# Performance work log

Hardware: AMD Instinct MI355X
Metric: run time of the kernel (lower is better)

The kernel has to match this reference:

```python
import jax, jax.numpy as jnp
import numpy as np


def setup_inputs() -> dict:
    key = jax.random.key(0)
    ks = jax.random.split(key, 6)
    B, N, D, H, W = 8, 16, 128, 64, 64
    x = jax.random.normal(ks[0], (B, N, D, H, W), dtype=jnp.float32)
    mask = jax.random.randint(ks[1], (B, N, H, W), 0, 2, dtype=jnp.int32)
    s = 1.0 / np.sqrt(D)
    Wq = jax.random.normal(ks[2], (D, D), dtype=jnp.float32) * s
    bq = jax.random.normal(ks[3], (D,), dtype=jnp.float32) * s
    Wk = jax.random.normal(ks[4], (D, D), dtype=jnp.float32) * s
    bk = jax.random.normal(ks[5], (D,), dtype=jnp.float32) * s
    return {"x": x, "mask": mask, "Wq": Wq, "bq": bq, "Wk": Wk, "bk": bk}


def reference(x, mask, Wq, bq, Wk, bk):
    B, N, D, H, W = x.shape
    K = H * W
    # (B, N, K, D) token view of spatial grid
    xr = jnp.transpose(x, (0, 1, 3, 4, 2)).reshape(B, N, K, D)
    m = mask.reshape(B, N, K, 1).astype(x.dtype)
    valid_count = jnp.sum(m, axis=2, keepdims=True)          # (B, N, 1, 1)
    mean_x = jnp.sum(xr * m, axis=2, keepdims=True) / valid_count  # (B, N, 1, D)
    # Linear layers: y = x @ W^T + b (torch convention)
    query = mean_x @ Wq.T + bq                               # (B, N, 1, D)
    keys = xr @ Wk.T + bk                                    # (B, N, K, D)
    attn = jnp.einsum('bnqd,bnkd->bnqk', query, keys)        # (B, N, 1, K)
    neg_inf = jnp.array(-jnp.inf, dtype=attn.dtype)
    attn = jnp.where(m.reshape(B, N, 1, K) == 0, neg_inf, attn)
    attn = jax.nn.softmax(attn / jnp.sqrt(jnp.asarray(D, attn.dtype)), axis=-1)
    pooled = jnp.einsum('bnqk,bnkd->bnqd', attn, xr)         # (B, N, 1, D)
    return pooled[:, :, 0, :]                                 # (B, N, D)
```

## Files before the change

### kernel.cpp

```cpp
#include <hip/hip_runtime.h>
#include <math.h>

#define G 128
#define D 128
#define K 4096
#define CK 64
#define PAD 1


__global__ __launch_bounds__(256) void k1_mean(const float* __restrict__ x,
                                               const int* __restrict__ mask,
                                               float* __restrict__ meanacc,
                                               float* __restrict__ oacc,
                                               float* __restrict__ denom) {
  __shared__ float mf[K];
  const int g = blockIdx.x >> 5;
  const int s = blockIdx.x & 31;
  const int tid = threadIdx.x;
  if (s == 0) {
    if (tid < D) oacc[g * D + tid] = 0.0f;
    if (tid == D) denom[g] = 0.0f;
  }
  const int4* m4 = (const int4*)(mask + (size_t)g * K);
  for (int i = tid; i < K / 4; i += 256) {
    int4 mi = m4[i];
    *(float4*)&mf[4 * i] =
        make_float4((float)mi.x, (float)mi.y, (float)mi.z, (float)mi.w);
  }
  __syncthreads();
  const int wid = tid >> 6, lane = tid & 63;
  const int d = s * 4 + wid;
  const float4* x4 = (const float4*)(x + ((size_t)g * D + d) * K);
  const float4* mf4 = (const float4*)mf;
  float4 acc = make_float4(0.f, 0.f, 0.f, 0.f);
#pragma unroll
  for (int it = 0; it < K / 256; ++it) {
    float4 a = x4[it * 64 + lane];
    float4 m = mf4[it * 64 + lane];
    acc.x += a.x * m.x;
    acc.y += a.y * m.y;
    acc.z += a.z * m.z;
    acc.w += a.w * m.w;
  }
  float sum = acc.x + acc.y + acc.z + acc.w;
#pragma unroll
  for (int o = 32; o > 0; o >>= 1) sum += __shfl_down(sum, o, 64);
  if (lane == 0) meanacc[g * D + d] = sum;
}

__global__ __launch_bounds__(128) void k2_query(
    const float* __restrict__ meanacc, const int* __restrict__ mask,
    const float* __restrict__ Wq, const float* __restrict__ bq,
    const float* __restrict__ Wk, const float* __restrict__ bk,
    float* __restrict__ qt, float* __restrict__ cvec) {
  __shared__ float mean_s[D], query_s[D], red[D];
  const int g = blockIdx.x, t = threadIdx.x;
  const int4* m4 = (const int4*)(mask + (size_t)g * K);
  int csum = 0;
  for (int i = t; i < K / 4; i += 128) {
    int4 v = m4[i];
    csum += v.x + v.y + v.z + v.w;
  }
  red[t] = (float)csum;
  __syncthreads();
  for (int o = 64; o > 0; o >>= 1) {
    if (t < o) red[t] += red[t + o];
    __syncthreads();
  }
  const float cnt = red[0];
  mean_s[t] = meanacc[g * D + t] / cnt;
  __syncthreads();
  float q = bq[t];
  for (int d = 0; d < D; ++d) q += mean_s[d] * Wq[t * D + d];
  query_s[t] = q;
  __syncthreads();
  red[t] = q * bk[t];
  __syncthreads();
  for (int o = 64; o > 0; o >>= 1) {
    if (t < o) red[t] += red[t + o];
    __syncthreads();
  }
  if (t == 0) cvec[g] = red[0];
  float qq = 0.f;
  for (int d = 0; d < D; ++d) qq += query_s[d] * Wk[d * D + t];
  qt[g * D + t] = qq;
}

__global__ __launch_bounds__(256) void k3_fused(
    const float* __restrict__ x, const int* __restrict__ mask,
    const float* __restrict__ qt, const float* __restrict__ cvec,
    float* __restrict__ oacc, float* __restrict__ denom) {
  __shared__ float xs[D][CK + PAD];
  __shared__ float qs[D];
  __shared__ float part_l[4][CK];
  __shared__ float wsm[CK];
  __shared__ float red[256];
  const int g = blockIdx.x >> 6;
  const int k0 = (blockIdx.x & 63) * CK;
  const int tid = threadIdx.x;
  if (tid < D) qs[tid] = qt[g * D + tid];
  const float4* xg = (const float4*)(x + (size_t)g * D * K + k0);
  for (int i = tid; i < D * (CK / 4); i += 256) {
    int d = i >> 4, j = i & 15;
    float4 v = xg[(size_t)d * (K / 4) + j];
    xs[d][4 * j + 0] = v.x;
    xs[d][4 * j + 1] = v.y;
    xs[d][4 * j + 2] = v.z;
    xs[d][4 * j + 3] = v.w;
  }
  __syncthreads();
  {
    const int k = tid & 63, p = tid >> 6;
    float s = 0.f;
#pragma unroll 8
    for (int d = p * 32; d < p * 32 + 32; ++d) s += qs[d] * xs[d][k];
    part_l[p][k] = s;
  }
  __syncthreads();
  if (tid < CK) {
    const float scale = 0.08838834764831845f;
    float l = (part_l[0][tid] + part_l[1][tid] + part_l[2][tid] +
               part_l[3][tid] + cvec[g]) * scale;
    float w = mask[(size_t)g * K + k0 + tid] ? __expf(l) : 0.f;
    wsm[tid] = w;
#pragma unroll
    for (int o = 32; o > 0; o >>= 1) w += __shfl_down(w, o, 64);
    if (tid == 0) atomicAdd(denom + g, w);
  }
  __syncthreads();
  {
    const int d = tid & 127, h = tid >> 7;
    float a = 0.f;
#pragma unroll 8
    for (int i = h * 32; i < h * 32 + 32; ++i) a += wsm[i] * xs[d][i];
    red[tid] = a;
  }
  __syncthreads();
  if (tid < D) atomicAdd(oacc + g * D + tid, red[tid] + red[tid + 128]);
}

__global__ __launch_bounds__(256) void k4_norm(const float* __restrict__ oacc,
                                               const float* __restrict__ denom,
                                               float* __restrict__ out) {
  int i = blockIdx.x * 256 + threadIdx.x;
  out[i] = oacc[i] / denom[i >> 7];
}

extern "C" void kernel_launch(void* const* d_in, const int* in_sizes, int n_in,
                              void* d_out, int out_size, void* d_ws,
                              size_t ws_size, hipStream_t stream) {
  const float* x = (const float*)d_in[0];
  const int* mask = (const int*)d_in[1];
  const float* Wq = (const float*)d_in[2];
  const float* bq = (const float*)d_in[3];
  const float* Wk = (const float*)d_in[4];
  const float* bk = (const float*)d_in[5];
  float* out = (float*)d_out;

  float* ws = (float*)d_ws;
  float* meanacc = ws;
  float* qt = ws + G * D;
  float* cvec = ws + 2 * G * D;
  float* oacc = ws + 2 * G * D + G;
  float* denom = ws + 3 * G * D + G;

  k1_mean<<<G * 32, 256, 0, stream>>>(x, mask, meanacc, oacc, denom);
  k2_query<<<G, 128, 0, stream>>>(meanacc, mask, Wq, bq, Wk, bk, qt, cvec);
  k3_fused<<<G * (K / CK), 256, 0, stream>>>(x, mask, qt, cvec, oacc, denom);
  k4_norm<<<(G * D) / 256, 256, 0, stream>>>(oacc, denom, out);
}
```

Baseline: 449.1 us.

## Fuse all four stages into one persistent cooperative kernel with work-stealing counters

Replaces the four separate launches with one persistent cooperative kernel. Blocks claim work items from atomic counters: first the masked mean reduction, then the per-group query projection run by the last finisher of each group, then the chunked attention-pooling items, which spin on a per-group ready flag. The last chunk of each group writes the normalized output. This removes kernel launch gaps and the separate normalize pass, and lets the phases of different groups overlap. In exchange it adds atomic and spin-wait overhead, a memset, and an occupancy query on the host on every launch.

```diff
diff --git a/kernel.cpp b/kernel.cpp
--- a/kernel.cpp
+++ b/kernel.cpp
@@ -5,145 +5,194 @@
 #define D 128
 #define K 4096
 #define CK 64
-#define PAD 1
-
-
-__global__ __launch_bounds__(256) void k1_mean(const float* __restrict__ x,
-                                               const int* __restrict__ mask,
-                                               float* __restrict__ meanacc,
-                                               float* __restrict__ oacc,
-                                               float* __restrict__ denom) {
-  __shared__ float mf[K];
-  const int g = blockIdx.x >> 5;
-  const int s = blockIdx.x & 31;
-  const int tid = threadIdx.x;
-  if (s == 0) {
-    if (tid < D) oacc[g * D + tid] = 0.0f;
-    if (tid == D) denom[g] = 0.0f;
-  }
-  const int4* m4 = (const int4*)(mask + (size_t)g * K);
-  for (int i = tid; i < K / 4; i += 256) {
-    int4 mi = m4[i];
-    *(float4*)&mf[4 * i] =
-        make_float4((float)mi.x, (float)mi.y, (float)mi.z, (float)mi.w);
-  }
-  __syncthreads();
-  const int wid = tid >> 6, lane = tid & 63;
-  const int d = s * 4 + wid;
-  const float4* x4 = (const float4*)(x + ((size_t)g * D + d) * K);
-  const float4* mf4 = (const float4*)mf;
-  float4 acc = make_float4(0.f, 0.f, 0.f, 0.f);
-#pragma unroll
-  for (int it = 0; it < K / 256; ++it) {
-    float4 a = x4[it * 64 + lane];
-    float4 m = mf4[it * 64 + lane];
-    acc.x += a.x * m.x;
-    acc.y += a.y * m.y;
-    acc.z += a.z * m.z;
-    acc.w += a.w * m.w;
-  }
-  float sum = acc.x + acc.y + acc.z + acc.w;
-#pragma unroll
-  for (int o = 32; o > 0; o >>= 1) sum += __shfl_down(sum, o, 64);
-  if (lane == 0) meanacc[g * D + d] = sum;
-}
-
-__global__ __launch_bounds__(128) void k2_query(
-    const float* __restrict__ meanacc, const int* __restrict__ mask,
+#define ITEMS_A (G * 32)
+#define ITEMS_B (G * 64)
+#define NBLK_MAX 1024
+
+#define LOADC(p) __hip_atomic_load((p), __ATOMIC_ACQUIRE, __HIP_MEMORY_SCOPE_AGENT)
+#define STOREC(p, v) \
+  __hip_atomic_store((p), (v), __ATOMIC_RELEASE, __HIP_MEMORY_SCOPE_AGENT)
+
+union SMem {
+  struct {
+    float mean_s[D];
+    float query_s[D];
+    float red2[256];
+  } a;
+  struct {
+    float xs[D][CK + 1];
+    float qs[D];
+    float part_l[4][CK];
+    float wsm[CK];
+    float red[256];
+  } b;
+};
+
+__global__ __launch_bounds__(256, 4) void fused_all(
+    const float* __restrict__ x, const int* __restrict__ mask,
     const float* __restrict__ Wq, const float* __restrict__ bq,
     const float* __restrict__ Wk, const float* __restrict__ bk,
-    float* __restrict__ qt, float* __restrict__ cvec) {
-  __shared__ float mean_s[D], query_s[D], red[D];
-  const int g = blockIdx.x, t = threadIdx.x;
-  const int4* m4 = (const int4*)(mask + (size_t)g * K);
-  int csum = 0;
-  for (int i = t; i < K / 4; i += 128) {
-    int4 v = m4[i];
-    csum += v.x + v.y + v.z + v.w;
+    float* meanacc, float* qt, float* cvec, float* oacc, float* denomv,
+    int* ctrl, float* out) {
+  __shared__ SMem sm;
+  __shared__ int s_claim, s_old;
+  __shared__ float s_cv;
+  int* doneA = ctrl;
+  int* doneB = ctrl + G;
+  int* ready = ctrl + 2 * G;
+  int* ctrA = ctrl + 3 * G;
+  int* ctrB = ctrl + 3 * G + 1;
+  const int tid = threadIdx.x;
+  const int wid = tid >> 6, lane = tid & 63;
+
+  for (;;) {
+    __syncthreads();
+    if (tid == 0)
+      s_claim = __hip_atomic_fetch_add(ctrA, 1, __ATOMIC_ACQ_REL,
+                                       __HIP_MEMORY_SCOPE_AGENT);
+    __syncthreads();
+    const int item = s_claim;
+    if (item >= ITEMS_A) break;
+    const int g = item >> 5, s = item & 31;
+    const int d = s * 4 + wid;
+    const float4* x4 = (const float4*)(x + ((size_t)g * D + d) * K);
+    const int4* m4 = (const int4*)(mask + (size_t)g * K);
+    float4 acc = make_float4(0.f, 0.f, 0.f, 0.f);
+#pragma unroll
+    for (int it = 0; it < K / 256; ++it) {
+      float4 a = x4[it * 64 + lane];
+      int4 mi = m4[it * 64 + lane];
+      acc.x += a.x * (float)mi.x;
+      acc.y += a.y * (float)mi.y;
+      acc.z += a.z * (float)mi.z;
+      acc.w += a.w * (float)mi.w;
+    }
+    float sum = acc.x + acc.y + acc.z + acc.w;
+#pragma unroll
+    for (int o = 32; o > 0; o >>= 1) sum += __shfl_down(sum, o, 64);
+    if (lane == 0) STOREC(meanacc + g * D + d, sum);
+    __syncthreads();
+    if (tid == 0)
+      s_old = __hip_atomic_fetch_add(doneA + g, 1, __ATOMIC_ACQ_REL,
+                                     __HIP_MEMORY_SCOPE_AGENT);
+    __syncthreads();
+    if (s_old == 31) {
+      {
+        const int4* mr = (const int4*)(mask + (size_t)g * K);
+        int cs = 0;
+#pragma unroll
+        for (int i = 0; i < 4; ++i) {
+          int4 v = mr[tid * 4 + i];
+          cs += v.x + v.y + v.z + v.w;
+        }
+        sm.a.red2[tid] = (float)cs;
+      }
+      __syncthreads();
+      for (int o = 128; o > 0; o >>= 1) {
+        if (tid < o) sm.a.red2[tid] += sm.a.red2[tid + o];
+        __syncthreads();
+      }
+      const float cnt = sm.a.red2[0];
+      if (tid < D) sm.a.mean_s[tid] = LOADC(meanacc + g * D + tid) / cnt;
+      __syncthreads();
+      if (tid < D) {
+        float q = bq[tid];
+        for (int dd = 0; dd < D; ++dd) q += sm.a.mean_s[dd] * Wq[tid * D + dd];
+        sm.a.query_s[tid] = q;
+      }
+      __syncthreads();
+      if (tid < D) sm.a.red2[tid] = sm.a.query_s[tid] * bk[tid];
+      else sm.a.red2[tid] = 0.f;
+      __syncthreads();
+      for (int o = 128; o > 0; o >>= 1) {
+        if (tid < o) sm.a.red2[tid] += sm.a.red2[tid + o];
+        __syncthreads();
+      }
+      if (tid == 0) STOREC(cvec + g, sm.a.red2[0]);
+      if (tid < D) {
+        float qq = 0.f;
+        for (int dd = 0; dd < D; ++dd) qq += sm.a.query_s[dd] * Wk[dd * D + tid];
+        STOREC(qt + g * D + tid, qq);
+        STOREC(oacc + g * D + tid, 0.0f);
+      }
+      if (tid == 0) STOREC(denomv + g, 0.0f);
+      __syncthreads();
+      if (tid == 0)
+        __hip_atomic_store(ready + g, 1, __ATOMIC_RELEASE,
+                           __HIP_MEMORY_SCOPE_AGENT);
+    }
   }
-  red[t] = (float)csum;
-  __syncthreads();
-  for (int o = 64; o > 0; o >>= 1) {
-    if (t < o) red[t] += red[t + o];
-    __syncthreads();
+
+  for (;;) {
+    __syncthreads();
+    if (tid == 0)
+      s_claim = __hip_atomic_fetch_add(ctrB, 1, __ATOMIC_ACQ_REL,
+                                       __HIP_MEMORY_SCOPE_AGENT);
+    __syncthreads();
+    const int item = s_claim;
+    if (item >= ITEMS_B) break;
+    const int g = item >> 6, k0 = (item & 63) * CK;
+    if (tid == 0) {
+      while (__hip_atomic_load(ready + g, __ATOMIC_ACQUIRE,
+                               __HIP_MEMORY_SCOPE_AGENT) == 0)
+        __builtin_amdgcn_s_sleep(8);
+      s_cv = LOADC(cvec + g);
+    }
+    __syncthreads();
+    if (tid < D) sm.b.qs[tid] = LOADC(qt + g * D + tid);
+    const float4* xg = (const float4*)(x + (size_t)g * D * K + k0);
+    for (int i = tid; i < D * (CK / 4); i += 256) {
+      int dd = i >> 4, j = i & 15;
+      float4 v = xg[(size_t)dd * (K / 4) + j];
+      sm.b.xs[dd][4 * j + 0] = v.x;
+      sm.b.xs[dd][4 * j + 1] = v.y;
+      sm.b.xs[dd][4 * j + 2] = v.z;
+      sm.b.xs[dd][4 * j + 3] = v.w;
+    }
+    __syncthreads();
+    {
+      const int k = tid & 63, p = tid >> 6;
+      float sp = 0.f;
+#pragma unroll 8
+      for (int dd = p * 32; dd < p * 32 + 32; ++dd)
+        sp += sm.b.qs[dd] * sm.b.xs[dd][k];
+      sm.b.part_l[p][k] = sp;
+    }
+    __syncthreads();
+    if (tid < CK) {
+      const float scale = 0.08838834764831845f;
+      float l = (sm.b.part_l[0][tid] + sm.b.part_l[1][tid] +
+                 sm.b.part_l[2][tid] + sm.b.part_l[3][tid] + s_cv) * scale;
+      float w = mask[(size_t)g * K + k0 + tid] ? __expf(l) : 0.f;
+      sm.b.wsm[tid] = w;
+#pragma unroll
+      for (int o = 32; o > 0; o >>= 1) w += __shfl_down(w, o, 64);
+      if (tid == 0) atomicAdd(denomv + g, w);
+    }
+    __syncthreads();
+    {
+      const int dd = tid & 127, h = tid >> 7;
+      float a2 = 0.f;
+#pragma unroll 8
+      for (int i = h * 32; i < h * 32 + 32; ++i)
+        a2 += sm.b.wsm[i] * sm.b.xs[dd][i];
+      sm.b.red[tid] = a2;
+    }
+    __syncthreads();
+    if (tid < D) atomicAdd(oacc + g * D + tid, sm.b.red[tid] + sm.b.red[tid + 128]);
+    __syncthreads();
+    if (tid == 0)
+      s_old = __hip_atomic_fetch_add(doneB + g, 1, __ATOMIC_ACQ_REL,
+                                     __HIP_MEMORY_SCOPE_AGENT);
+    __syncthreads();
+    if (s_old == 63) {
+      if (tid < D) {
+        float o = LOADC(oacc + g * D + tid);
+        float den = LOADC(denomv + g);
+        out[g * D + tid] = o / den;
+      }
+    }
   }
-  const float cnt = red[0];
-  mean_s[t] = meanacc[g * D + t] / cnt;
-  __syncthreads();
-  float q = bq[t];
-  for (int d = 0; d < D; ++d) q += mean_s[d] * Wq[t * D + d];
-  query_s[t] = q;
-  __syncthreads();
-  red[t] = q * bk[t];
-  __syncthreads();
-  for (int o = 64; o > 0; o >>= 1) {
-    if (t < o) red[t] += red[t + o];
-    __syncthreads();
-  }
-  if (t == 0) cvec[g] = red[0];
-  float qq = 0.f;
-  for (int d = 0; d < D; ++d) qq += query_s[d] * Wk[d * D + t];
-  qt[g * D + t] = qq;
-}
-
-__global__ __launch_bounds__(256) void k3_fused(
-    const float* __restrict__ x, const int* __restrict__ mask,
-    const float* __restrict__ qt, const float* __restrict__ cvec,
-    float* __restrict__ oacc, float* __restrict__ denom) {
-  __shared__ float xs[D][CK + PAD];
-  __shared__ float qs[D];
-  __shared__ float part_l[4][CK];
-  __shared__ float wsm[CK];
-  __shared__ float red[256];
-  const int g = blockIdx.x >> 6;
-  const int k0 = (blockIdx.x & 63) * CK;
-  const int tid = threadIdx.x;
-  if (tid < D) qs[tid] = qt[g * D + tid];
-  const float4* xg = (const float4*)(x + (size_t)g * D * K + k0);
-  for (int i = tid; i < D * (CK / 4); i += 256) {
-    int d = i >> 4, j = i & 15;
-    float4 v = xg[(size_t)d * (K / 4) + j];
-    xs[d][4 * j + 0] = v.x;
-    xs[d][4 * j + 1] = v.y;
-    xs[d][4 * j + 2] = v.z;
-    xs[d][4 * j + 3] = v.w;
-  }
-  __syncthreads();
-  {
-    const int k = tid & 63, p = tid >> 6;
-    float s = 0.f;
-#pragma unroll 8
-    for (int d = p * 32; d < p * 32 + 32; ++d) s += qs[d] * xs[d][k];
-    part_l[p][k] = s;
-  }
-  __syncthreads();
-  if (tid < CK) {
-    const float scale = 0.08838834764831845f;
-    float l = (part_l[0][tid] + part_l[1][tid] + part_l[2][tid] +
-               part_l[3][tid] + cvec[g]) * scale;
-    float w = mask[(size_t)g * K + k0 + tid] ? __expf(l) : 0.f;
-    wsm[tid] = w;
-#pragma unroll
-    for (int o = 32; o > 0; o >>= 1) w += __shfl_down(w, o, 64);
-    if (tid == 0) atomicAdd(denom + g, w);
-  }
-  __syncthreads();
-  {
-    const int d = tid & 127, h = tid >> 7;
-    float a = 0.f;
-#pragma unroll 8
-    for (int i = h * 32; i < h * 32 + 32; ++i) a += wsm[i] * xs[d][i];
-    red[tid] = a;
-  }
-  __syncthreads();
-  if (tid < D) atomicAdd(oacc + g * D + tid, red[tid] + red[tid + 128]);
-}
-
-__global__ __launch_bounds__(256) void k4_norm(const float* __restrict__ oacc,
-                                               const float* __restrict__ denom,
-                                               float* __restrict__ out) {
-  int i = blockIdx.x * 256 + threadIdx.x;
-  out[i] = oacc[i] / denom[i >> 7];
 }
 
 extern "C" void kernel_launch(void* const* d_in, const int* in_sizes, int n_in,
@@ -162,10 +211,22 @@
   float* qt = ws + G * D;
   float* cvec = ws + 2 * G * D;
   float* oacc = ws + 2 * G * D + G;
-  float* denom = ws + 3 * G * D + G;
-
-  k1_mean<<<G * 32, 256, 0, stream>>>(x, mask, meanacc, oacc, denom);
-  k2_query<<<G, 128, 0, stream>>>(meanacc, mask, Wq, bq, Wk, bk, qt, cvec);
-  k3_fused<<<G * (K / CK), 256, 0, stream>>>(x, mask, qt, cvec, oacc, denom);
-  k4_norm<<<(G * D) / 256, 256, 0, stream>>>(oacc, denom, out);
+  float* denomv = ws + 3 * G * D + G;
+  int* ctrl = (int*)(ws + 3 * G * D + 2 * G);
+
+  hipMemsetAsync(ctrl, 0, (3 * G + 2) * sizeof(int), stream);
+
+  int perCU = 0;
+  hipOccupancyMaxActiveBlocksPerMultiprocessor(&perCU, (const void*)fused_all,
+                                               256, 0);
+  if (perCU < 1) perCU = 1;
+  int grid = perCU * 256;
+  if (grid > NBLK_MAX) grid = NBLK_MAX;
+
+  void* args[] = {(void*)&x,    (void*)&mask, (void*)&Wq,     (void*)&bq,
+                  (void*)&Wk,   (void*)&bk,   (void*)&meanacc, (void*)&qt,
+                  (void*)&cvec, (void*)&oacc, (void*)&denomv, (void*)&ctrl,
+                  (void*)&out};
+  hipLaunchCooperativeKernel((const void*)fused_all, dim3(grid), dim3(256),
+                             args, 0, stream);
 }
```

New measurement: 1.552 ms. 245% more time.

## Fuse query projection and normalization into producer kernels via last-block counters

Applied to the files above, without the earlier changes.

The separate query kernel is folded into the mean kernel: the last block of each group, found through an atomic completion counter, computes the count, query, bias term and key-projected query. The separate normalization kernel is likewise folded into the attention-pooling kernel, where the last block per group divides by the denominator. This cuts the work from four launches to two plus a memset, removing launch gaps and tail serialization. In exchange each block pays an extra atomic and barriers, the memset is added, and the query work runs on one block per group at the tail.

```diff
diff --git a/kernel.cpp b/kernel.cpp
--- a/kernel.cpp
+++ b/kernel.cpp
@@ -5,21 +5,23 @@
 #define D 128
 #define K 4096
 #define CK 64
-#define PAD 1
 
-
-__global__ __launch_bounds__(256) void k1_mean(const float* __restrict__ x,
-                                               const int* __restrict__ mask,
-                                               float* __restrict__ meanacc,
-                                               float* __restrict__ oacc,
-                                               float* __restrict__ denom) {
+__global__ __launch_bounds__(256) void kA(
+    const float* __restrict__ x, const int* __restrict__ mask,
+    const float* __restrict__ Wq, const float* __restrict__ bq,
+    const float* __restrict__ Wk, const float* __restrict__ bk,
+    float* __restrict__ meanacc, float* __restrict__ qt,
+    float* __restrict__ cvec, float* __restrict__ oacc,
+    float* __restrict__ denomv, int* __restrict__ doneA) {
   __shared__ float mf[K];
-  const int g = blockIdx.x >> 5;
-  const int s = blockIdx.x & 31;
+  __shared__ float red[256];
+  __shared__ float mean_s[D], query_s[D];
+  __shared__ int s_old;
+  const int g = blockIdx.x >> 5, s = blockIdx.x & 31;
   const int tid = threadIdx.x;
   if (s == 0) {
     if (tid < D) oacc[g * D + tid] = 0.0f;
-    if (tid == D) denom[g] = 0.0f;
+    if (tid == D) denomv[g] = 0.0f;
   }
   const int4* m4 = (const int4*)(mask + (size_t)g * K);
   for (int i = tid; i < K / 4; i += 256) {
@@ -46,75 +48,76 @@
 #pragma unroll
   for (int o = 32; o > 0; o >>= 1) sum += __shfl_down(sum, o, 64);
   if (lane == 0) meanacc[g * D + d] = sum;
+  __syncthreads();
+  if (tid == 0)
+    s_old = __hip_atomic_fetch_add(doneA + g, 1, __ATOMIC_ACQ_REL,
+                                   __HIP_MEMORY_SCOPE_AGENT);
+  __syncthreads();
+  if (s_old == 31) {
+    float cs = 0.f;
+#pragma unroll
+    for (int i = 0; i < 16; ++i) cs += mf[i * 256 + tid];
+    red[tid] = cs;
+    __syncthreads();
+    for (int o = 128; o > 0; o >>= 1) {
+      if (tid < o) red[tid] += red[tid + o];
+      __syncthreads();
+    }
+    const float cnt = red[0];
+    if (tid < D) mean_s[tid] = meanacc[g * D + tid] / cnt;
+    __syncthreads();
+    if (tid < D) {
+      float q = bq[tid];
+      for (int dd = 0; dd < D; ++dd) q += mean_s[dd] * Wq[tid * D + dd];
+      query_s[tid] = q;
+    }
+    __syncthreads();
+    red[tid] = (tid < D) ? query_s[tid] * bk[tid] : 0.f;
+    __syncthreads();
+    for (int o = 128; o > 0; o >>= 1) {
+      if (tid < o) red[tid] += red[tid + o];
+      __syncthreads();
+    }
+    if (tid == 0) cvec[g] = red[0];
+    if (tid < D) {
+      float qq = 0.f;
+      for (int dd = 0; dd < D; ++dd) qq += query_s[dd] * Wk[dd * D + tid];
+      qt[g * D + tid] = qq;
+    }
+  }
 }
 
-__global__ __launch_bounds__(128) void k2_query(
-    const float* __restrict__ meanacc, const int* __restrict__ mask,
-    const float* __restrict__ Wq, const float* __restrict__ bq,
-    const float* __restrict__ Wk, const float* __restrict__ bk,
-    float* __restrict__ qt, float* __restrict__ cvec) {
-  __shared__ float mean_s[D], query_s[D], red[D];
-  const int g = blockIdx.x, t = threadIdx.x;
-  const int4* m4 = (const int4*)(mask + (size_t)g * K);
-  int csum = 0;
-  for (int i = t; i < K / 4; i += 128) {
-    int4 v = m4[i];
-    csum += v.x + v.y + v.z + v.w;
-  }
-  red[t] = (float)csum;
-  __syncthreads();
-  for (int o = 64; o > 0; o >>= 1) {
-    if (t < o) red[t] += red[t + o];
-    __syncthreads();
-  }
-  const float cnt = red[0];
-  mean_s[t] = meanacc[g * D + t] / cnt;
-  __syncthreads();
-  float q = bq[t];
-  for (int d = 0; d < D; ++d) q += mean_s[d] * Wq[t * D + d];
-  query_s[t] = q;
-  __syncthreads();
-  red[t] = q * bk[t];
-  __syncthreads();
-  for (int o = 64; o > 0; o >>= 1) {
-    if (t < o) red[t] += red[t + o];
-    __syncthreads();
-  }
-  if (t == 0) cvec[g] = red[0];
-  float qq = 0.f;
-  for (int d = 0; d < D; ++d) qq += query_s[d] * Wk[d * D + t];
-  qt[g * D + t] = qq;
-}
-
-__global__ __launch_bounds__(256) void k3_fused(
+__global__ __launch_bounds__(256) void kB(
     const float* __restrict__ x, const int* __restrict__ mask,
     const float* __restrict__ qt, const float* __restrict__ cvec,
-    float* __restrict__ oacc, float* __restrict__ denom) {
-  __shared__ float xs[D][CK + PAD];
+    float* __restrict__ oacc, float* __restrict__ denomv,
+    int* __restrict__ doneB, float* __restrict__ out) {
+  __shared__ float xs[D][CK + 1];
   __shared__ float qs[D];
   __shared__ float part_l[4][CK];
   __shared__ float wsm[CK];
   __shared__ float red[256];
+  __shared__ int s_old;
   const int g = blockIdx.x >> 6;
   const int k0 = (blockIdx.x & 63) * CK;
   const int tid = threadIdx.x;
   if (tid < D) qs[tid] = qt[g * D + tid];
   const float4* xg = (const float4*)(x + (size_t)g * D * K + k0);
   for (int i = tid; i < D * (CK / 4); i += 256) {
-    int d = i >> 4, j = i & 15;
-    float4 v = xg[(size_t)d * (K / 4) + j];
-    xs[d][4 * j + 0] = v.x;
-    xs[d][4 * j + 1] = v.y;
-    xs[d][4 * j + 2] = v.z;
-    xs[d][4 * j + 3] = v.w;
+    int dd = i >> 4, j = i & 15;
+    float4 v = xg[(size_t)dd * (K / 4) + j];
+    xs[dd][4 * j + 0] = v.x;
+    xs[dd][4 * j + 1] = v.y;
+    xs[dd][4 * j + 2] = v.z;
+    xs[dd][4 * j + 3] = v.w;
   }
   __syncthreads();
   {
     const int k = tid & 63, p = tid >> 6;
-    float s = 0.f;
+    float sp = 0.f;
 #pragma unroll 8
-    for (int d = p * 32; d < p * 32 + 32; ++d) s += qs[d] * xs[d][k];
-    part_l[p][k] = s;
+    for (int dd = p * 32; dd < p * 32 + 32; ++dd) sp += qs[dd] * xs[dd][k];
+    part_l[p][k] = sp;
   }
   __syncthreads();
   if (tid < CK) {
@@ -125,25 +128,27 @@
     wsm[tid] = w;
 #pragma unroll
     for (int o = 32; o > 0; o >>= 1) w += __shfl_down(w, o, 64);
-    if (tid == 0) atomicAdd(denom + g, w);
+    if (tid == 0) atomicAdd(denomv + g, w);
   }
   __syncthreads();
   {
-    const int d = tid & 127, h = tid >> 7;
-    float a = 0.f;
+    const int dd = tid & 127, h = tid >> 7;
+    float a2 = 0.f;
 #pragma unroll 8
-    for (int i = h * 32; i < h * 32 + 32; ++i) a += wsm[i] * xs[d][i];
-    red[tid] = a;
+    for (int i = h * 32; i < h * 32 + 32; ++i) a2 += wsm[i] * xs[dd][i];
+    red[tid] = a2;
   }
   __syncthreads();
-  if (tid < D) atomicAdd(oacc + g * D + tid, red[tid] + red[tid + 128]);
-}
-
-__global__ __launch_bounds__(256) void k4_norm(const float* __restrict__ oacc,
-                                               const float* __restrict__ denom,
-                                               float* __restrict__ out) {
-  int i = blockIdx.x * 256 + threadIdx.x;
-  out[i] = oacc[i] / denom[i >> 7];
+  if (tid < D)
+    atomicAdd(oacc + g * D + tid, red[tid] + red[tid + 128]);
+  __syncthreads();
+  if (tid == 0)
+    s_old = __hip_atomic_fetch_add(doneB + g, 1, __ATOMIC_ACQ_REL,
+                                   __HIP_MEMORY_SCOPE_AGENT);
+  __syncthreads();
+  if (s_old == 63) {
+    if (tid < D) out[g * D + tid] = oacc[g * D + tid] / denomv[g];
+  }
 }
 
 extern "C" void kernel_launch(void* const* d_in, const int* in_sizes, int n_in,
@@ -162,10 +167,12 @@
   float* qt = ws + G * D;
   float* cvec = ws + 2 * G * D;
   float* oacc = ws + 2 * G * D + G;
-  float* denom = ws + 3 * G * D + G;
+  float* denomv = ws + 3 * G * D + G;
+  int* doneA = (int*)(ws + 3 * G * D + 2 * G);
+  int* doneB = doneA + G;
 
-  k1_mean<<<G * 32, 256, 0, stream>>>(x, mask, meanacc, oacc, denom);
-  k2_query<<<G, 128, 0, stream>>>(meanacc, mask, Wq, bq, Wk, bk, qt, cvec);
-  k3_fused<<<G * (K / CK), 256, 0, stream>>>(x, mask, qt, cvec, oacc, denom);
-  k4_norm<<<(G * D) / 256, 256, 0, stream>>>(oacc, denom, out);
+  hipMemsetAsync(doneA, 0, 2 * G * sizeof(int), stream);
+  kA<<<G * 32, 256, 0, stream>>>(x, mask, Wq, bq, Wk, bk, meanacc, qt, cvec,
+                                 oacc, denomv, doneA);
+  kB<<<G * 64, 256, 0, stream>>>(x, mask, qt, cvec, oacc, denomv, doneB, out);
 }
```

Measured after the change: 807.3 us. 79.8% more time.
